# Kernel tuning notes

Measured on AMD Instinct MI355X. Metric: run time of the kernel, lower is better.

## Reference

```python
import jax, jax.numpy as jnp
import numpy as np
from jax import lax

PAD = 4  # conv padding (kernel_size=9, stride=1 -> same length)
ITERATIONS = 3


def _squash(x):
    # squash along last dim: scale = |x|^2/(1+|x|^2), out = scale * x/|x|
    norm = jnp.sqrt(jnp.sum(x * x, axis=-1, keepdims=True))
    scale = norm ** 2 / (1.0 + norm ** 2)
    return scale * x / norm


def setup_inputs() -> dict:
    key = jax.random.key(0)
    ks = jax.random.split(key, 6)
    B, IC, L = 16, 16, 4096
    OC, NC, CD, K = 256, 8, 16, 9
    return {
        "x": jax.random.normal(ks[0], (B, IC, L), dtype=jnp.float32),
        "conv_w": jax.random.normal(ks[1], (OC, IC, K), dtype=jnp.float32) * 0.05,
        "conv_b": jax.random.normal(ks[2], (OC,), dtype=jnp.float32) * 0.05,
        "caps_w": jax.random.normal(ks[3], (NC, CD, OC), dtype=jnp.float32) * 0.05,
        "caps_b": jax.random.normal(ks[4], (NC, CD), dtype=jnp.float32) * 0.05,
        "W": jax.random.normal(ks[5], (NC, IC, CD, 1, 1), dtype=jnp.float32),
    }


def reference(x, conv_w, conv_b, caps_w, caps_b, W):
    # conv_layer: Conv1d(IC -> OC, k=9, stride=1, pad=4)
    y = lax.conv_general_dilated(
        x, conv_w, window_strides=(1,), padding=[(PAD, PAD)],
        dimension_numbers=("NCH", "OIH", "NCH"),
    ) + conv_b[None, :, None]                      # [B, OC, S]

    # primary capsules: NC independent 1x1 convs OC->CD, stacked.
    # u[b, k, n, s] = sum_c y[b, c, s] * caps_w[n, k, c] + caps_b[n, k]
    u = jnp.einsum("bcs,nkc->bkns", y, caps_w) + caps_b.T[None, :, :, None]  # [B, CD, NC, S]

    u_hat = lax.stop_gradient(u)  # u.detach()
    v = None
    for i in range(ITERATIONS):
        c = jax.nn.softmax(W, axis=1)                     # [NC, IC, CD, 1, 1]
        # broadcast: c [NC, IC, CD, 1, 1] * u_hat [(NC,) B, CD, NC, S] (IC == B)
        s = jnp.sum(c * u_hat, axis=1, keepdims=True)     # [NC, 1, CD, NC, S]
        v = _squash(s)
        if i < ITERATIONS - 1:
            u_hat = u + v * jnp.sum(u * s, axis=1, keepdims=True)  # [NC, B, CD, NC, S]
    return jnp.squeeze(v, axis=1)                         # [NC, CD, NC, S]
```

## Files before the change

### kernel.cpp

```cpp
#include <hip/hip_runtime.h>
#include <hip/hip_bf16.h>
#include <stdint.h>

#define IK_ 144
typedef __fp16 h2 __attribute__((ext_vector_type(2)));

#define WS_CWH 0u
#define WS_CB  10240u
#define WS_U   10368u

__device__ __forceinline__ uint32_t pack2bf(float a, float b) {
    const uint32_t lo = (uint32_t)__bfloat16_as_ushort(__float2bfloat16(a));
    const uint32_t hi = (uint32_t)__bfloat16_as_ushort(__float2bfloat16(b));
    return lo | (hi << 16);
}
#define BFLO(u) __uint_as_float((u) << 16)
#define BFHI(u) __uint_as_float((u) & 0xffff0000u)

__global__ void k_cw(const float* __restrict__ caps_w,
                     const float* __restrict__ conv_w,
                     const float* __restrict__ conv_b,
                     const float* __restrict__ caps_b,
                     float* __restrict__ ws) {
    __shared__ float cwl[256];
    __shared__ float cwf[IK_];
    const int nk  = blockIdx.x;
    const int tid = threadIdx.x;
    cwl[tid] = caps_w[nk*256 + tid];
    __syncthreads();
    if (tid < IK_) {
        float a0 = 0.f, a1 = 0.f, a2 = 0.f, a3 = 0.f;
        for (int c = 0; c < 256; c += 4) {
            a0 += cwl[c+0] * conv_w[(c+0)*IK_ + tid];
            a1 += cwl[c+1] * conv_w[(c+1)*IK_ + tid];
            a2 += cwl[c+2] * conv_w[(c+2)*IK_ + tid];
            a3 += cwl[c+3] * conv_w[(c+3)*IK_ + tid];
        }
        cwf[tid] = (a0 + a1) + (a2 + a3);
    } else if (tid == IK_) {
        float a = 0.f;
        for (int c = 0; c < 256; ++c) a += cwl[c] * conv_b[c];
        ws[WS_CB + nk] = a + caps_b[nk];
    }
    __syncthreads();
    if (tid < 80) {
        const int i = tid / 5, p = tid - 5*i;
        const float w0 = cwf[i*9 + 2*p];
        const float w1 = (p < 4) ? cwf[i*9 + 2*p + 1] : 0.f;
        const h2 hp = __builtin_amdgcn_cvt_pkrtz(w0, w1);
        ((uint32_t*)ws)[WS_CWH + (((nk >> 3)*16 + i)*5 + p)*8 + (nk & 7)] =
            __builtin_bit_cast(uint32_t, hp);
    }
}

__global__ void __launch_bounds__(256) k_conv(const float* __restrict__ x,
                                              const float* __restrict__ wsc,
                                              float* __restrict__ ws) {
    const int tid   = threadIdx.x;
    const int b     = blockIdx.x & 15;
    const int oct   = (blockIdx.x >> 4) & 7;
    const int stile = blockIdx.x >> 7;
    const int sbase = stile << 9;

    __shared__ float xs[16*528];

    {
        const int row = tid >> 4;
        const int c0  = tid & 15;
        const float* xr = x + (b << 16) + (row << 12);
        float* lr = xs + row*528;
        #pragma unroll
        for (int k9 = 0; k9 < 9; ++k9) {
            const int col = c0 + (k9 << 4);
            if (col < 131) {
                const int j0 = sbase - 4 + (col << 2);
                float4 v;
                if (j0 < 0 || j0 > 4092) v = make_float4(0.f, 0.f, 0.f, 0.f);
                else v = *(const float4*)(xr + j0);
                *(float4*)(lr + (col << 2)) = v;
            }
        }
    }
    __syncthreads();

    const int sid = tid & 127;
    const int g   = __builtin_amdgcn_readfirstlane(oct*2 + (tid >> 7));
    const uint32_t* __restrict__ cwp = (const uint32_t*)wsc + WS_CWH + g*640;
    const float*    __restrict__ cbp = wsc + WS_CB + (g << 3);

    float4 acc[8];
    #pragma unroll
    for (int q = 0; q < 8; ++q) acc[q] = make_float4(0.f, 0.f, 0.f, 0.f);

    #pragma unroll
    for (int c4 = 0; c4 < 4; ++c4) {
        float4 w[4][4];
        #pragma unroll
        for (int ii = 0; ii < 4; ++ii) {
            const float* rw = xs + (c4*4 + ii)*528 + (sid << 2);
            w[ii][0] = ((const float4*)rw)[0];
            w[ii][1] = ((const float4*)rw)[1];
            w[ii][2] = ((const float4*)rw)[2];
            w[ii][3] = ((const float4*)rw)[3];
        }
        #pragma unroll
        for (int ii = 0; ii < 4; ++ii) {
            const int i = c4*4 + ii;
            const float f[14] = {w[ii][0].x,w[ii][0].y,w[ii][0].z,w[ii][0].w,
                                 w[ii][1].x,w[ii][1].y,w[ii][1].z,w[ii][1].w,
                                 w[ii][2].x,w[ii][2].y,w[ii][2].z,w[ii][2].w,
                                 w[ii][3].x,w[ii][3].y};
            h2 E[6], O[6];
            #pragma unroll
            for (int d = 0; d < 6; ++d) {
                E[d] = __builtin_amdgcn_cvt_pkrtz(f[2*d],   f[2*d+1]);
                O[d] = __builtin_amdgcn_cvt_pkrtz(f[2*d+1], f[2*d+2]);
            }
            const uint32_t* cpi = cwp + i*40;
            #pragma unroll
            for (int q = 0; q < 8; ++q) {
                #pragma unroll
                for (int p = 0; p < 5; ++p) {
                    const h2 wv = __builtin_bit_cast(h2, cpi[p*8 + q]);
                    acc[q].x = __builtin_amdgcn_fdot2(wv, E[p],   acc[q].x, false);
                    acc[q].y = __builtin_amdgcn_fdot2(wv, O[p],   acc[q].y, false);
                    acc[q].z = __builtin_amdgcn_fdot2(wv, E[p+1], acc[q].z, false);
                    acc[q].w = __builtin_amdgcn_fdot2(wv, O[p+1], acc[q].w, false);
                }
            }
        }
    }

    const int s = sbase + (sid << 2);
    uint16_t* up = (uint16_t*)(ws + WS_U);
    #pragma unroll
    for (int q = 0; q < 8; ++q) {
        const int nk = (g << 3) + q;
        const float cbv = cbp[q];
        const uint32_t p0 = pack2bf(acc[q].x + cbv, acc[q].y + cbv);
        const uint32_t p1 = pack2bf(acc[q].z + cbv, acc[q].w + cbv);
        *(uint2*)(up + (((size_t)((b << 7) + nk)) << 12) + s) = make_uint2(p0, p1);
    }
}

__device__ __forceinline__ float block_sum(float v, float* red, int tid) {
    #pragma unroll
    for (int off = 32; off; off >>= 1) v += __shfl_down(v, off, 64);
    if ((tid & 63) == 0) red[tid >> 6] = v;
    __syncthreads();
    const float r = (red[0] + red[1]) + (red[2] + red[3]);
    __syncthreads();
    return r;
}

__global__ void __launch_bounds__(256) k_route(const float* __restrict__ wsc,
                                               const float* __restrict__ W,
                                               float* __restrict__ out) {
    const int tid = threadIdx.x;
    const int nk  = blockIdx.x & 127;
    const int m   = blockIdx.x >> 7;
    const int n   = nk >> 4, k = nk & 15;
    __shared__ float wl[16];
    __shared__ float red[4];
    if (tid < 16) wl[tid] = W[m*256 + tid*16 + k];
    __syncthreads();

    float c[16], mx = -1e30f;
    #pragma unroll
    for (int b = 0; b < 16; ++b) { c[b] = wl[b]; mx = fmaxf(mx, c[b]); }
    float sum = 0.f;
    #pragma unroll
    for (int b = 0; b < 16; ++b) { c[b] = __expf(c[b] - mx); sum += c[b]; }
    const float inv = 1.f / sum;
    #pragma unroll
    for (int b = 0; b < 16; ++b) c[b] *= inv;

    float sv[16], Uv[16];
    #pragma unroll
    for (int j = 0; j < 16; ++j) { sv[j] = 0.f; Uv[j] = 0.f; }
    const uint16_t* ub = (const uint16_t*)(wsc + WS_U) + ((size_t)nk << 12) + (tid << 4);
    for (int b = 0; b < 16; ++b) {
        const uint16_t* p16 = ub + ((size_t)b << 19);
        const uint4 va = *(const uint4*)(p16);
        const uint4 vb = *(const uint4*)(p16 + 8);
        float uv[16];
        uv[0]=BFLO(va.x);  uv[1]=BFHI(va.x);  uv[2]=BFLO(va.y);  uv[3]=BFHI(va.y);
        uv[4]=BFLO(va.z);  uv[5]=BFHI(va.z);  uv[6]=BFLO(va.w);  uv[7]=BFHI(va.w);
        uv[8]=BFLO(vb.x);  uv[9]=BFHI(vb.x);  uv[10]=BFLO(vb.y); uv[11]=BFHI(vb.y);
        uv[12]=BFLO(vb.z); uv[13]=BFHI(vb.z); uv[14]=BFLO(vb.w); uv[15]=BFHI(vb.w);
        const float cb_ = c[b];
        #pragma unroll
        for (int j = 0; j < 16; ++j) {
            Uv[j] += uv[j];
            sv[j]  = fmaf(cb_, uv[j], sv[j]);
        }
    }

    float p = 0.f;
    #pragma unroll
    for (int j = 0; j < 16; ++j) p = fmaf(sv[j], sv[j], p);
    const float n0 = block_sum(p, red, tid);
    const float r0 = __fsqrt_rn(n0) / (1.f + n0);

    float s1[16];
    p = 0.f;
    #pragma unroll
    for (int j = 0; j < 16; ++j) {
        s1[j] = sv[j] * fmaf(r0*sv[j], Uv[j], 1.f);
        p = fmaf(s1[j], s1[j], p);
    }
    const float n1 = block_sum(p, red, tid);
    const float r1 = __fsqrt_rn(n1) / (1.f + n1);

    p = 0.f;
    #pragma unroll
    for (int j = 0; j < 16; ++j) {
        s1[j] = fmaf(r1*s1[j]*s1[j], Uv[j], sv[j]);
        p = fmaf(s1[j], s1[j], p);
    }
    const float n2 = block_sum(p, red, tid);
    const float r2 = __fsqrt_rn(n2) / (1.f + n2);

    float4* po = (float4*)(out + ((size_t)((m*16 + k)*8 + n) << 12) + (tid << 4));
    #pragma unroll
    for (int q = 0; q < 4; ++q)
        po[q] = make_float4(s1[4*q+0]*r2, s1[4*q+1]*r2, s1[4*q+2]*r2, s1[4*q+3]*r2);
}

extern "C" void kernel_launch(void* const* d_in, const int* in_sizes, int n_in,
                              void* d_out, int out_size, void* d_ws, size_t ws_size,
                              hipStream_t stream) {
    const float* x      = (const float*)d_in[0];
    const float* conv_w = (const float*)d_in[1];
    const float* conv_b = (const float*)d_in[2];
    const float* caps_w = (const float*)d_in[3];
    const float* caps_b = (const float*)d_in[4];
    const float* W      = (const float*)d_in[5];
    float* ws  = (float*)d_ws;
    float* out = (float*)d_out;

    hipLaunchKernelGGL(k_cw,    dim3(128),  dim3(256), 0, stream, caps_w, conv_w, conv_b, caps_b, ws);
    hipLaunchKernelGGL(k_conv,  dim3(1024), dim3(256), 0, stream, x, ws, ws);
    hipLaunchKernelGGL(k_route, dim3(1024), dim3(256), 0, stream, ws, W, out);
}
```

Baseline: 121.9 us.

## Rewrite fused conv-capsule projection as fp16 MFMA implicit GEMM

```diff
diff --git a/kernel.cpp b/kernel.cpp
--- a/kernel.cpp
+++ b/kernel.cpp
@@ -3,7 +3,9 @@
 #include <stdint.h>
 
 #define IK_ 144
-typedef __fp16 h2 __attribute__((ext_vector_type(2)));
+typedef __fp16 h2    __attribute__((ext_vector_type(2)));
+typedef __fp16 f16x8 __attribute__((ext_vector_type(8)));
+typedef float  f32x4 __attribute__((ext_vector_type(4)));
 
 #define WS_CWH 0u
 #define WS_CB  10240u
@@ -43,13 +45,11 @@
         ws[WS_CB + nk] = a + caps_b[nk];
     }
     __syncthreads();
-    if (tid < 80) {
-        const int i = tid / 5, p = tid - 5*i;
-        const float w0 = cwf[i*9 + 2*p];
-        const float w1 = (p < 4) ? cwf[i*9 + 2*p + 1] : 0.f;
-        const h2 hp = __builtin_amdgcn_cvt_pkrtz(w0, w1);
-        ((uint32_t*)ws)[WS_CWH + (((nk >> 3)*16 + i)*5 + p)*8 + (nk & 7)] =
-            __builtin_bit_cast(uint32_t, hp);
+    if (tid < 160) {
+        const int i = tid / 10;
+        const int t = tid - 10*i;
+        const float v = (t < 9) ? cwf[i*9 + t] : 0.f;
+        ((uint16_t*)(ws + WS_CWH))[nk*160 + tid] = __builtin_bit_cast(uint16_t, (__fp16)v);
     }
 }
 
@@ -58,21 +58,30 @@
                                               float* __restrict__ ws) {
     const int tid   = threadIdx.x;
     const int b     = blockIdx.x & 15;
-    const int oct   = (blockIdx.x >> 4) & 7;
-    const int stile = blockIdx.x >> 7;
-    const int sbase = stile << 9;
-
-    __shared__ float xs[16*528];
+    const int stile = blockIdx.x >> 4;
+    const int sbase = stile << 7;
+
+    __shared__ float  xs[16*140];
+    __shared__ __fp16 aw[128*168];
+    __shared__ float  cbl[128];
 
     {
-        const int row = tid >> 4;
-        const int c0  = tid & 15;
+        const int row = tid >> 1, hf = tid & 1;
+        const uint4* src = (const uint4*)((const uint16_t*)(wsc + WS_CWH) + row*160 + hf*80);
+        uint4* dst = (uint4*)(aw + row*168 + hf*80);
+        #pragma unroll
+        for (int j = 0; j < 10; ++j) dst[j] = src[j];
+    }
+    if (tid < 128) cbl[tid] = wsc[WS_CB + tid];
+
+    {
+        const int row = tid >> 4, c0 = tid & 15;
         const float* xr = x + (b << 16) + (row << 12);
-        float* lr = xs + row*528;
-        #pragma unroll
-        for (int k9 = 0; k9 < 9; ++k9) {
-            const int col = c0 + (k9 << 4);
-            if (col < 131) {
+        float* lr = xs + row*140;
+        #pragma unroll
+        for (int k3 = 0; k3 < 3; ++k3) {
+            const int col = c0 + (k3 << 4);
+            if (col < 35) {
                 const int j0 = sbase - 4 + (col << 2);
                 float4 v;
                 if (j0 < 0 || j0 > 4092) v = make_float4(0.f, 0.f, 0.f, 0.f);
@@ -83,63 +92,76 @@
     }
     __syncthreads();
 
-    const int sid = tid & 127;
-    const int g   = __builtin_amdgcn_readfirstlane(oct*2 + (tid >> 7));
-    const uint32_t* __restrict__ cwp = (const uint32_t*)wsc + WS_CWH + g*640;
-    const float*    __restrict__ cbp = wsc + WS_CB + (g << 3);
-
-    float4 acc[8];
-    #pragma unroll
-    for (int q = 0; q < 8; ++q) acc[q] = make_float4(0.f, 0.f, 0.f, 0.f);
-
-    #pragma unroll
-    for (int c4 = 0; c4 < 4; ++c4) {
-        float4 w[4][4];
-        #pragma unroll
-        for (int ii = 0; ii < 4; ++ii) {
-            const float* rw = xs + (c4*4 + ii)*528 + (sid << 2);
-            w[ii][0] = ((const float4*)rw)[0];
-            w[ii][1] = ((const float4*)rw)[1];
-            w[ii][2] = ((const float4*)rw)[2];
-            w[ii][3] = ((const float4*)rw)[3];
-        }
-        #pragma unroll
-        for (int ii = 0; ii < 4; ++ii) {
-            const int i = c4*4 + ii;
-            const float f[14] = {w[ii][0].x,w[ii][0].y,w[ii][0].z,w[ii][0].w,
-                                 w[ii][1].x,w[ii][1].y,w[ii][1].z,w[ii][1].w,
-                                 w[ii][2].x,w[ii][2].y,w[ii][2].z,w[ii][2].w,
-                                 w[ii][3].x,w[ii][3].y};
-            h2 E[6], O[6];
+    const int lane = tid & 63;
+    const int wid  = tid >> 6;
+    const int sub  = lane & 15;
+    const int g    = lane >> 4;
+    const int wm   = wid >> 1;
+    const int wn   = wid & 1;
+
+    f32x4 acc[4][4] = {};
+
+    #pragma unroll
+    for (int kb = 0; kb < 5; ++kb) {
+        f16x8 a[4];
+        #pragma unroll
+        for (int mi = 0; mi < 4; ++mi)
+            a[mi] = *(const f16x8*)(aw + ((wm<<6) + (mi<<4) + sub)*168 + (kb<<5) + (g<<3));
+
+        int offs[8];
+        #pragma unroll
+        for (int e = 0; e < 8; ++e) {
+            const int kp = (kb<<5) + (g<<3) + e;
+            const int i  = kp / 10;
+            offs[e] = i*140 + (kp - 10*i);
+        }
+
+        f16x8 bf[4];
+        #pragma unroll
+        for (int ni = 0; ni < 4; ++ni) {
+            const int sl = (wn<<6) + (ni<<4) + sub;
+            float f[8];
             #pragma unroll
-            for (int d = 0; d < 6; ++d) {
-                E[d] = __builtin_amdgcn_cvt_pkrtz(f[2*d],   f[2*d+1]);
-                O[d] = __builtin_amdgcn_cvt_pkrtz(f[2*d+1], f[2*d+2]);
-            }
-            const uint32_t* cpi = cwp + i*40;
+            for (int e = 0; e < 8; ++e) f[e] = xs[offs[e] + sl];
+            union { h2 h[4]; f16x8 v; } u;
+            u.h[0] = __builtin_amdgcn_cvt_pkrtz(f[0], f[1]);
+            u.h[1] = __builtin_amdgcn_cvt_pkrtz(f[2], f[3]);
+            u.h[2] = __builtin_amdgcn_cvt_pkrtz(f[4], f[5]);
+            u.h[3] = __builtin_amdgcn_cvt_pkrtz(f[6], f[7]);
+            bf[ni] = u.v;
+        }
+
+        #pragma unroll
+        for (int mi = 0; mi < 4; ++mi) {
             #pragma unroll
-            for (int q = 0; q < 8; ++q) {
-                #pragma unroll
-                for (int p = 0; p < 5; ++p) {
-                    const h2 wv = __builtin_bit_cast(h2, cpi[p*8 + q]);
-                    acc[q].x = __builtin_amdgcn_fdot2(wv, E[p],   acc[q].x, false);
-                    acc[q].y = __builtin_amdgcn_fdot2(wv, O[p],   acc[q].y, false);
-                    acc[q].z = __builtin_amdgcn_fdot2(wv, E[p+1], acc[q].z, false);
-                    acc[q].w = __builtin_amdgcn_fdot2(wv, O[p+1], acc[q].w, false);
-                }
-            }
-        }
-    }
-
-    const int s = sbase + (sid << 2);
-    uint16_t* up = (uint16_t*)(ws + WS_U);
-    #pragma unroll
-    for (int q = 0; q < 8; ++q) {
-        const int nk = (g << 3) + q;
-        const float cbv = cbp[q];
-        const uint32_t p0 = pack2bf(acc[q].x + cbv, acc[q].y + cbv);
-        const uint32_t p1 = pack2bf(acc[q].z + cbv, acc[q].w + cbv);
-        *(uint2*)(up + (((size_t)((b << 7) + nk)) << 12) + s) = make_uint2(p0, p1);
+            for (int ni = 0; ni < 4; ++ni)
+                acc[mi][ni] = __builtin_amdgcn_mfma_f32_16x16x32_f16(a[mi], bf[ni], acc[mi][ni], 0, 0, 0);
+        }
+    }
+
+    const int odd = sub & 1;
+    uint32_t* uw = (uint32_t*)((uint16_t*)(ws + WS_U));
+    #pragma unroll
+    for (int mi = 0; mi < 4; ++mi) {
+        const int nkb = (wm<<6) + (mi<<4) + (g<<2);
+        const float cb0 = cbl[nkb+0], cb1 = cbl[nkb+1], cb2 = cbl[nkb+2], cb3 = cbl[nkb+3];
+        #pragma unroll
+        for (int ni = 0; ni < 4; ++ni) {
+            const f32x4 v = acc[mi][ni];
+            const uint32_t A01 = pack2bf(v.x + cb0, v.y + cb1);
+            const uint32_t A23 = pack2bf(v.z + cb2, v.w + cb3);
+            const uint32_t Q01 = (uint32_t)__shfl_xor((int)A01, 1);
+            const uint32_t Q23 = (uint32_t)__shfl_xor((int)A23, 1);
+            const uint32_t dA = odd ? ((Q01 >> 16) | (A01 & 0xffff0000u))
+                                    : ((A01 & 0xffffu) | (Q01 << 16));
+            const uint32_t dB = odd ? ((Q23 >> 16) | (A23 & 0xffff0000u))
+                                    : ((A23 & 0xffffu) | (Q23 << 16));
+            const int nkA = nkb + odd;
+            const int s0  = sbase + (wn<<6) + (ni<<4) + (sub & ~1);
+            const size_t di = (((size_t)((b<<7) + nkA)) << 11) + (s0 >> 1);
+            uw[di]        = dA;
+            uw[di + 4096] = dB;
+        }
     }
 }
 
@@ -240,6 +262,6 @@
     float* out = (float*)d_out;
 
     hipLaunchKernelGGL(k_cw,    dim3(128),  dim3(256), 0, stream, caps_w, conv_w, conv_b, caps_b, ws);
-    hipLaunchKernelGGL(k_conv,  dim3(1024), dim3(256), 0, stream, x, ws, ws);
+    hipLaunchKernelGGL(k_conv,  dim3(512),  dim3(256), 0, stream, x, ws, ws);
     hipLaunchKernelGGL(k_route, dim3(1024), dim3(256), 0, stream, ws, W, out);
 }
```

After: 107.0 us. -12.2%, faster.
